# Kernel tuning notes

Hardware: AMD Instinct MI355X
Metric: run time of the kernel (lower is better)

## Reference

```python
import jax, jax.numpy as jnp
import numpy as np

N_EMBED = 384
N_HEAD = 6
HEAD_SIZE = N_EMBED // N_HEAD  # 64
LN_EPS = 1e-5


def setup_inputs() -> dict:
    key = jax.random.key(0)
    ks = jax.random.split(key, 12)
    B, T = 128, 256
    s_in = 1.0 / np.sqrt(N_EMBED)
    s_ff = 1.0 / np.sqrt(4 * N_EMBED)
    return {
        "x": jax.random.normal(ks[0], (B, T, N_EMBED), jnp.float32),
        "Wq": jax.random.normal(ks[1], (N_HEAD, N_EMBED, HEAD_SIZE), jnp.float32) * s_in,
        "Wk": jax.random.normal(ks[2], (N_HEAD, N_EMBED, HEAD_SIZE), jnp.float32) * s_in,
        "Wv": jax.random.normal(ks[3], (N_HEAD, N_EMBED, HEAD_SIZE), jnp.float32) * s_in,
        "Wproj": jax.random.normal(ks[4], (N_EMBED, N_EMBED), jnp.float32) * s_in,
        "bproj": jnp.zeros((N_EMBED,), jnp.float32),
        "W1": jax.random.normal(ks[5], (N_EMBED, 4 * N_EMBED), jnp.float32) * s_in,
        "b1": jnp.zeros((4 * N_EMBED,), jnp.float32),
        "W2": jax.random.normal(ks[6], (4 * N_EMBED, N_EMBED), jnp.float32) * s_ff,
        "b2": jnp.zeros((N_EMBED,), jnp.float32),
        "ln1_g": jnp.ones((N_EMBED,), jnp.float32),
        "ln1_b": jnp.zeros((N_EMBED,), jnp.float32),
        "ln2_g": jnp.ones((N_EMBED,), jnp.float32),
        "ln2_b": jnp.zeros((N_EMBED,), jnp.float32),
    }


def _layernorm(x, g, b):
    mu = jnp.mean(x, axis=-1, keepdims=True)
    var = jnp.mean(jnp.square(x - mu), axis=-1, keepdims=True)
    return (x - mu) * jax.lax.rsqrt(var + LN_EPS) * g + b


def _attention(xn, Wq, Wk, Wv, Wproj, bproj):
    B, T, C = xn.shape
    q = jnp.einsum("btc,hcd->bhtd", xn, Wq)
    k = jnp.einsum("btc,hcd->bhtd", xn, Wk)
    v = jnp.einsum("btc,hcd->bhtd", xn, Wv)
    # NOTE: original scales by C**-0.5 with C = n_embed (384), not head_size
    scores = jnp.einsum("bhtd,bhsd->bhts", q, k) * (C ** -0.5)
    causal = jnp.tril(jnp.ones((T, T), bool))
    scores = jnp.where(causal, scores, -jnp.inf)
    wei = jax.nn.softmax(scores, axis=-1)
    out = jnp.einsum("bhts,bhsd->bhtd", wei, v)
    out = out.transpose(0, 2, 1, 3).reshape(B, T, N_EMBED)  # concat heads
    return out @ Wproj + bproj


def reference(x, Wq, Wk, Wv, Wproj, bproj, W1, b1, W2, b2, ln1_g, ln1_b, ln2_g, ln2_b):
    x = x + _attention(_layernorm(x, ln1_g, ln1_b), Wq, Wk, Wv, Wproj, bproj)
    h = _layernorm(x, ln2_g, ln2_b)
    ff = jax.nn.relu(h @ W1 + b1) @ W2 + b2
    return x + ff
```

## Files before the change

### kernel.cpp

```cpp
#include <hip/hip_runtime.h>
#include <hip/hip_bf16.h>

typedef __hip_bfloat16 bf16;
typedef __attribute__((ext_vector_type(8))) short bf16x8;
typedef __attribute__((ext_vector_type(4))) float f32x4;

#define CEMB 384
#define NHEAD 6
#define HSZ 64
#define TSEQ 256
#define BATCH 128
#define MROWS (BATCH*TSEQ)
#define FDIM 1536
#define QSCALE 0.05103103630798288f
#define SMAX 8.0f

#define AS1 __attribute__((address_space(1)))
#define AS3 __attribute__((address_space(3)))
__device__ __forceinline__ void gload16(const void* g, void* l){
  __builtin_amdgcn_global_load_lds((const AS1 unsigned*)(g), (AS3 unsigned*)(l), 16, 0, 0);
}

__global__ __launch_bounds__(256) void ln_kernel(const float* __restrict__ x,
    const float* __restrict__ gam, const float* __restrict__ bet,
    bf16* __restrict__ y)
{
  const int row  = blockIdx.x*4 + (threadIdx.x>>6);
  const int lane = threadIdx.x & 63;
  const float* xr = x + (size_t)row*CEMB;
  float v[6]; float s = 0.f;
  #pragma unroll
  for (int i=0;i<6;i++){ v[i] = xr[lane + i*64]; s += v[i]; }
  #pragma unroll
  for (int m=1;m<64;m<<=1) s += __shfl_xor(s, m, 64);
  const float mu = s * (1.0f/CEMB);
  float qs = 0.f;
  #pragma unroll
  for (int i=0;i<6;i++){ v[i] -= mu; qs += v[i]*v[i]; }
  #pragma unroll
  for (int m=1;m<64;m<<=1) qs += __shfl_xor(qs, m, 64);
  const float rs = rsqrtf(qs*(1.0f/CEMB) + 1e-5f);
  bf16* yr = y + (size_t)row*CEMB;
  #pragma unroll
  for (int i=0;i<6;i++){
    int c = lane + i*64;
    yr[c] = __float2bfloat16(v[i]*rs*gam[c] + bet[c]);
  }
}

__global__ __launch_bounds__(256) void transpose_to_bf16(const float* __restrict__ src,
    bf16* __restrict__ dst, int K, int N)
{
  __shared__ float tile[32][33];
  const int n0 = blockIdx.x*32, k0 = blockIdx.y*32;
  src += (size_t)blockIdx.z*K*N;
  dst += (size_t)blockIdx.z*K*N;
  const int c = threadIdx.x & 31, r8 = threadIdx.x >> 5;
  #pragma unroll
  for (int i=0;i<4;i++)
    tile[r8 + i*8][c] = src[(size_t)(k0 + r8 + i*8)*N + n0 + c];
  __syncthreads();
  #pragma unroll
  for (int i=0;i<4;i++)
    dst[(size_t)(n0 + r8 + i*8)*K + k0 + c] = __float2bfloat16(tile[c][r8 + i*8]);
}

__global__ __launch_bounds__(256) void transpose_qkv(const float* __restrict__ Wq,
    const float* __restrict__ Wk, const float* __restrict__ Wv, bf16* __restrict__ dst)
{
  __shared__ float tile[32][33];
  const int z = blockIdx.z;
  const float* src = (z < 6) ? Wq : (z < 12 ? Wk : Wv);
  src += (size_t)(z % 6) * CEMB * HSZ;
  dst += (size_t)z * CEMB * HSZ;
  const int n0 = blockIdx.x*32, k0 = blockIdx.y*32;
  const int c = threadIdx.x & 31, r8 = threadIdx.x >> 5;
  #pragma unroll
  for (int i=0;i<4;i++)
    tile[r8 + i*8][c] = src[(size_t)(k0 + r8 + i*8)*HSZ + n0 + c];
  __syncthreads();
  #pragma unroll
  for (int i=0;i<4;i++)
    dst[(size_t)(n0 + r8 + i*8)*CEMB + k0 + c] = __float2bfloat16(tile[c][r8 + i*8]);
}

template<int EPI, int NN, int NK>
__global__ __launch_bounds__(512) void gemm2(
    const bf16* __restrict__ A, const bf16* __restrict__ BT,
    const float* __restrict__ bias, const float* __restrict__ resid,
    float* __restrict__ outf, bf16* __restrict__ outb0,
    bf16* __restrict__ outb1, bf16* __restrict__ outb2)
{
  constexpr int K = NK*32;
  constexpr int N = NN*128;
  __shared__ char lA[2][256*64];
  __shared__ char lB[2][128*64];
  const int cpx = gridDim.x >> 3;
  const int wg  = (blockIdx.x & 7)*cpx + (blockIdx.x >> 3);
  const int bm = (wg / NN)*256, bn = (wg % NN)*128;
  const int t = threadIdx.x, lane = t & 63, wid = t >> 6;
  const int wr = (wid>>1)*64, wc = (wid&1)*64;
  const int g = lane >> 4, fr = lane & 15;
  const size_t rowK2 = (size_t)K*2;
  f32x4 acc[4][4] = {};

  auto stage = [&](int buf, int kt){
    const size_t ko = (size_t)kt*64;
    #pragma unroll
    for (int i=0;i<2;i++){
      int slot = t + i*512;
      int row = slot>>2, blk = slot&3;
      gload16((const char*)A + (size_t)(bm+row)*rowK2 + ko + ((blk ^ ((row>>1)&3))<<4),
              lA[buf] + slot*16);
    }
    {
      int row = t>>2, blk = t&3;
      gload16((const char*)BT + (size_t)(bn+row)*rowK2 + ko + ((blk ^ ((row>>1)&3))<<4),
              lB[buf] + t*16);
    }
  };

  stage(0, 0);
  __syncthreads();
  int cur = 0;
  #pragma unroll 1
  for (int kt=0; kt<NK; ++kt){
    if (kt+1 < NK) stage(cur^1, kt+1);
    bf16x8 af[4], bq[4];
    #pragma unroll
    for (int mi=0;mi<4;mi++){
      int row = wr + mi*16 + fr;
      af[mi] = *(const bf16x8*)(lA[cur] + row*64 + ((g ^ ((row>>1)&3))<<4));
    }
    #pragma unroll
    for (int nj=0;nj<4;nj++){
      int row = wc + nj*16 + fr;
      bq[nj] = *(const bf16x8*)(lB[cur] + row*64 + ((g ^ ((row>>1)&3))<<4));
    }
    __builtin_amdgcn_s_setprio(1);
    #pragma unroll
    for (int mi=0;mi<4;mi++)
      #pragma unroll
      for (int nj=0;nj<4;nj++)
        acc[mi][nj] = __builtin_amdgcn_mfma_f32_16x16x32_bf16(af[mi], bq[nj], acc[mi][nj], 0, 0, 0);
    __builtin_amdgcn_s_setprio(0);
    __syncthreads();
    cur ^= 1;
  }

  if constexpr (EPI==0){
    const int sel = bn/CEMB;
    bf16* dst = sel==0 ? outb0 : (sel==1 ? outb1 : outb2);
    const float sc = sel==0 ? QSCALE : 1.0f;
    const int nb = bn - sel*CEMB;
    #pragma unroll
    for (int nj=0;nj<4;nj++){
      const int nn = nb + wc + nj*16 + fr;
      const int hh = nn>>6, dd = nn&63;
      #pragma unroll
      for (int mi=0;mi<4;mi++){
        const int m0 = bm + wr + mi*16 + 4*g;
        const int bb = m0>>8, tt0 = m0&255;
        bf16* p = dst + ((size_t)(bb*NHEAD + hh)*TSEQ + tt0)*HSZ + dd;
        #pragma unroll
        for (int e=0;e<4;e++)
          p[(size_t)e*HSZ] = __float2bfloat16(acc[mi][nj][e]*sc);
      }
    }
  } else {
    #pragma unroll
    for (int mi=0;mi<4;mi++)
      #pragma unroll
      for (int nj=0;nj<4;nj++)
        #pragma unroll
        for (int e=0;e<4;e++){
          const int m = bm + wr + mi*16 + 4*g + e;
          const int n = bn + wc + nj*16 + fr;
          const float vacc = acc[mi][nj][e];
          if constexpr (EPI==1 || EPI==3){
            outf[(size_t)m*N + n] = vacc + bias[n] + resid[(size_t)m*N + n];
          } else {
            float z = vacc + bias[n];
            outb0[(size_t)m*N + n] = __float2bfloat16(z > 0.f ? z : 0.f);
          }
        }
  }
}

__global__ __launch_bounds__(256) void attn_kernel(
    const bf16* __restrict__ q, const bf16* __restrict__ k,
    const bf16* __restrict__ v, bf16* __restrict__ out)
{
  __shared__ char kt_lds[64*128];
  __shared__ char vt_lds[80*128];
  __shared__ char p_lds[4][64*128];
  const int bh = blockIdx.x;
  const int bidx = bh / NHEAD, hidx = bh - bidx*NHEAD;
  const int t = threadIdx.x, lane = t & 63, w = t >> 6;
  const int g = lane >> 4, fr = lane & 15;
  const int lrow = lane >> 3;
  const int scol = ((lane & 7) ^ lrow) << 4;
  const size_t base = (size_t)bh * TSEQ * HSZ;

  if (t < 128){
    unsigned int ones2 = 0x3F803F80u;
    uint4 vv;
    if ((t>>3) == 0) vv = uint4{ones2, ones2, ones2, ones2};
    else             vv = uint4{0u, 0u, 0u, 0u};
    *(uint4*)(vt_lds + (64 + (t>>3))*128 + (t&7)*16) = vv;
  }

  bf16x8 qf[4][2];
  #pragma unroll
  for (int mi=0;mi<4;mi++)
    #pragma unroll
    for (int ks=0;ks<2;ks++)
      qf[mi][ks] = *(const bf16x8*)(q + base + (size_t)(w*64 + mi*16 + fr)*HSZ + ks*32 + g*8);

  f32x4 of[4][5] = {};

  for (int j=0;j<4;j++){
    __syncthreads();
    #pragma unroll
    for (int i=0;i<2;i++){
      int r0 = w*16 + i*8;
      gload16((const char*)(k + base + (size_t)(j*64 + r0 + lrow)*HSZ) + scol,
              kt_lds + r0*128);
    }
    #pragma unroll
    for (int i=0;i<2;i++){
      int chunk = t + i*256, r = chunk>>3, c = chunk&7;
      uint4 vv = *(const uint4*)(v + base + (size_t)(j*64 + r)*HSZ + c*8);
      const unsigned short* pv = (const unsigned short*)&vv;
      #pragma unroll
      for (int u=0;u<8;u++)
        *(unsigned short*)(vt_lds + (c*8+u)*128 + ((((r>>3) ^ u ^ c)&7)<<4) + (r&7)*2) = pv[u];
    }
    __syncthreads();
    if (j <= w){
      f32x4 sa[4][4] = {};
      #pragma unroll
      for (int ks=0;ks<2;ks++){
        bf16x8 kf[4];
        #pragma unroll
        for (int nj=0;nj<4;nj++)
          kf[nj] = *(const bf16x8*)(kt_lds + (nj*16+fr)*128 + (((ks*4+g)*16) ^ ((fr&7)<<4)));
        __builtin_amdgcn_s_setprio(1);
        #pragma unroll
        for (int mi=0;mi<4;mi++)
          #pragma unroll
          for (int nj=0;nj<4;nj++)
            sa[mi][nj] = __builtin_amdgcn_mfma_f32_16x16x32_bf16(qf[mi][ks], kf[nj], sa[mi][nj], 0, 0, 0);
        __builtin_amdgcn_s_setprio(0);
      }
      if (j == w){
        #pragma unroll
        for (int mi=0;mi<4;mi++)
          #pragma unroll
          for (int nj=0;nj<4;nj++)
            #pragma unroll
            for (int e=0;e<4;e++)
              if (nj*16 + fr > mi*16 + 4*g + e) sa[mi][nj][e] = -1e30f;
      }
      char* pl = p_lds[w];
      #pragma unroll
      for (int mi=0;mi<4;mi++)
        #pragma unroll
        for (int nj=0;nj<4;nj++)
          #pragma unroll
          for (int e=0;e<4;e++){
            int row = mi*16 + 4*g + e, col = nj*16 + fr;
            float p = __expf(sa[mi][nj][e] - SMAX);
            *(bf16*)(pl + row*128 + (((col>>3) ^ (row&7))<<4) + (col&7)*2) =
                __float2bfloat16(p);
          }
      #pragma unroll
      for (int ks=0;ks<2;ks++){
        bf16x8 pa[4], vf[5];
        #pragma unroll
        for (int mi=0;mi<4;mi++)
          pa[mi] = *(const bf16x8*)(pl + (mi*16+fr)*128 + (((ks*4+g)*16) ^ ((fr&7)<<4)));
        #pragma unroll
        for (int nd=0;nd<5;nd++){
          int d = nd*16 + fr;
          vf[nd] = *(const bf16x8*)(vt_lds + d*128 +
                   ((((ks*4+g) ^ (d&7) ^ ((d>>3)&7))&7)<<4));
        }
        __builtin_amdgcn_s_setprio(1);
        #pragma unroll
        for (int mi=0;mi<4;mi++)
          #pragma unroll
          for (int nd=0;nd<5;nd++)
            of[mi][nd] = __builtin_amdgcn_mfma_f32_16x16x32_bf16(pa[mi], vf[nd], of[mi][nd], 0, 0, 0);
        __builtin_amdgcn_s_setprio(0);
      }
    }
  }
  #pragma unroll
  for (int mi=0;mi<4;mi++){
    float rl[4];
    #pragma unroll
    for (int e=0;e<4;e++){
      float l = __shfl(of[mi][4][e], (int)(lane & 48), 64);
      rl[e] = 1.0f / l;
    }
    #pragma unroll
    for (int nd=0;nd<4;nd++)
      #pragma unroll
      for (int e=0;e<4;e++){
        int row = w*64 + mi*16 + 4*g + e;
        int d = nd*16 + fr;
        out[(size_t)(bidx*TSEQ + row)*CEMB + hidx*HSZ + d] =
            __float2bfloat16(of[mi][nd][e] * rl[e]);
      }
  }
}

extern "C" void kernel_launch(void* const* d_in, const int* in_sizes, int n_in,
                              void* d_out, int out_size, void* d_ws, size_t ws_size,
                              hipStream_t stream)
{
  const float* x     = (const float*)d_in[0];
  const float* Wq    = (const float*)d_in[1];
  const float* Wk    = (const float*)d_in[2];
  const float* Wv    = (const float*)d_in[3];
  const float* Wproj = (const float*)d_in[4];
  const float* bproj = (const float*)d_in[5];
  const float* W1    = (const float*)d_in[6];
  const float* b1    = (const float*)d_in[7];
  const float* W2    = (const float*)d_in[8];
  const float* b2    = (const float*)d_in[9];
  const float* ln1g  = (const float*)d_in[10];
  const float* ln1b  = (const float*)d_in[11];
  const float* ln2g  = (const float*)d_in[12];
  const float* ln2b  = (const float*)d_in[13];

  char* ws = (char*)d_ws;
  const size_t SA = (size_t)MROWS*CEMB*2;
  bf16* xn1    = (bf16*)(ws + 0*SA);
  bf16* qb     = (bf16*)(ws + 1*SA);
  bf16* kbuf   = (bf16*)(ws + 2*SA);
  bf16* vb     = (bf16*)(ws + 3*SA);
  bf16* attn_o = (bf16*)(ws + 0*SA);
  bf16* act    = (bf16*)(ws + 0*SA);
  bf16* hb     = (bf16*)(ws + 4*SA);
  float* x1    = (float*)(ws + 5*SA);
  char* wb     = ws + 5*SA + (size_t)MROWS*CEMB*4;
  bf16* qkvT   = (bf16*)wb;
  bf16* projT  = (bf16*)(wb + (size_t)1152*384*2);
  bf16* w1T    = (bf16*)(wb + (size_t)(1152+384)*384*2);
  bf16* w2T    = (bf16*)(wb + (size_t)(1152+384+1536)*384*2);

  dim3 blk(256), blk5(512);
  transpose_qkv<<<dim3(2,12,18), blk, 0, stream>>>(Wq, Wk, Wv, qkvT);
  transpose_to_bf16<<<dim3(12,12,1), blk, 0, stream>>>(Wproj, projT, CEMB, CEMB);
  transpose_to_bf16<<<dim3(48,12,1), blk, 0, stream>>>(W1,    w1T,   CEMB, FDIM);
  transpose_to_bf16<<<dim3(12,48,1), blk, 0, stream>>>(W2,    w2T,   FDIM, CEMB);

  ln_kernel<<<dim3(MROWS/4), blk, 0, stream>>>(x, ln1g, ln1b, xn1);
  gemm2<0,9,12><<<dim3(1152), blk5, 0, stream>>>(xn1, qkvT, nullptr, nullptr,
                                                 nullptr, qb, kbuf, vb);
  attn_kernel<<<dim3(768), blk, 0, stream>>>(qb, kbuf, vb, attn_o);
  gemm2<1,3,12><<<dim3(384), blk5, 0, stream>>>(attn_o, projT, bproj, x,
                                                x1, nullptr, nullptr, nullptr);
  ln_kernel<<<dim3(MROWS/4), blk, 0, stream>>>(x1, ln2g, ln2b, hb);
  gemm2<2,12,12><<<dim3(1536), blk5, 0, stream>>>(hb, w1T, b1, nullptr,
                                                  nullptr, act, nullptr, nullptr);
  gemm2<3,3,48><<<dim3(384), blk5, 0, stream>>>(act, w2T, b2, x1,
                                                (float*)d_out, nullptr, nullptr, nullptr);
}
```

Measured before the change: 267.9 us.

## Add 256x256-tile GEMM with split-K-phase LDS pipeline for QKV, proj, FFN1

Introduces a new GEMM kernel with 256x256 output tiles and 8 waves, each computing 128x64. It uses a 128KB double-buffered LDS loaded by direct global-to-LDS loads, interleaving prefetch of the next K-slab with MFMA groups under explicit barriers and waitcnts. The QKV, projection and FFN1 GEMMs switch to it, with N padded to a multiple of 256 and padded columns masked in the epilogue. The aim is more operand reuse per LDS byte and better overlap of loads with MFMA. In exchange, the projection GEMM does wasted work on padding, the large LDS footprint limits occupancy, and the epilogue stores are less coalesced.

```diff
diff --git a/kernel.cpp b/kernel.cpp
--- a/kernel.cpp
+++ b/kernel.cpp
@@ -84,12 +84,133 @@
     dst[(size_t)(n0 + r8 + i*8)*CEMB + k0 + c] = __float2bfloat16(tile[c][r8 + i*8]);
 }
 
-template<int EPI, int NN, int NK>
-__global__ __launch_bounds__(512) void gemm2(
+template<int EPI, int NREAL, int NPAD, int NK>
+__global__ __launch_bounds__(512, 2) void gemm8p(
     const bf16* __restrict__ A, const bf16* __restrict__ BT,
     const float* __restrict__ bias, const float* __restrict__ resid,
     float* __restrict__ outf, bf16* __restrict__ outb0,
     bf16* __restrict__ outb1, bf16* __restrict__ outb2)
+{
+  constexpr int K = NK*64;
+  constexpr int NT = NPAD/256;
+  __shared__ char lds[131072];
+  const int cpx = gridDim.x >> 3;
+  const int wg  = (blockIdx.x & 7)*cpx + (blockIdx.x >> 3);
+  const int bm = (wg / NT)*256, bn = (wg % NT)*256;
+  const int t = threadIdx.x, lane = t & 63, wid = t >> 6;
+  const int wm = wid >> 2, wn = wid & 3;
+  const int g = lane >> 4, fr = lane & 15;
+  const size_t rowb = (size_t)K*2;
+  const int sblk = ((t&3) ^ ((t>>3)&3)) << 4;
+  const int swz  = (g ^ ((fr>>1)&3)) << 4;
+  f32x4 acc[8][4] = {};
+
+  const char* Ag = (const char*)A  + (size_t)(bm + (t>>2))*rowb + sblk;
+  const char* Bg = (const char*)BT + (size_t)(bn + (t>>2))*rowb + sblk;
+  const size_t rstep = rowb*128;
+
+  auto stg = [&](int X, int KH, int sl, int kt2){
+    const char* src = (X ? Bg : Ag) + (size_t)kt2*128 + KH*64;
+    char* dst = lds + X*65536 + (KH*2+sl)*16384 + wid*1024;
+    gload16(src,         dst);
+    gload16(src + rstep, dst + 8192);
+  };
+  auto rdA = [&](bf16x8* af, int sl, int MH, int KS){
+    const char* p = lds + (KS*2+sl)*16384 + (wm*128 + MH*64 + fr)*64 + swz;
+    #pragma unroll
+    for (int mi=0;mi<4;mi++) af[mi] = *(const bf16x8*)(p + mi*1024);
+  };
+  auto rdB = [&](bf16x8* bq, int sl, int KS){
+    const char* p = lds + 65536 + (KS*2+sl)*16384 + (wn*64 + fr)*64 + swz;
+    #pragma unroll
+    for (int nj=0;nj<4;nj++) bq[nj] = *(const bf16x8*)(p + nj*1024);
+  };
+
+#define MFMA16(MH) \
+  __builtin_amdgcn_s_setprio(1); \
+  _Pragma("unroll") \
+  for (int mi=0;mi<4;mi++){ \
+    _Pragma("unroll") \
+    for (int nj=0;nj<4;nj++) \
+      acc[(MH)*4+mi][nj] = __builtin_amdgcn_mfma_f32_16x16x32_bf16(af[mi], bq[nj], acc[(MH)*4+mi][nj], 0, 0, 0); \
+  } \
+  __builtin_amdgcn_s_setprio(0);
+
+  stg(0,0,0,0); stg(1,0,0,0); stg(0,1,0,0); stg(1,1,0,0);
+  asm volatile("s_waitcnt vmcnt(4)" ::: "memory");
+  __builtin_amdgcn_s_barrier();
+
+  #pragma unroll 1
+  for (int kt=0; kt<NK; ++kt){
+    const int sl = kt&1, sn = sl^1;
+    const bool pf = (kt+1 < NK);
+    bf16x8 af[4], bq[4];
+    rdA(af, sl, 0, 0); rdB(bq, sl, 0);
+    if (pf) stg(0,0,sn,kt+1);
+    __builtin_amdgcn_s_barrier();
+    asm volatile("s_waitcnt lgkmcnt(0)" ::: "memory");
+    __builtin_amdgcn_sched_barrier(0);
+    MFMA16(0)
+    __builtin_amdgcn_s_barrier();
+    rdA(af, sl, 1, 0);
+    if (pf){ stg(1,0,sn,kt+1);
+             asm volatile("s_waitcnt vmcnt(4)" ::: "memory"); }
+    else     asm volatile("s_waitcnt vmcnt(0)" ::: "memory");
+    __builtin_amdgcn_s_barrier();
+    asm volatile("s_waitcnt lgkmcnt(0)" ::: "memory");
+    __builtin_amdgcn_sched_barrier(0);
+    MFMA16(1)
+    __builtin_amdgcn_s_barrier();
+    rdA(af, sl, 0, 1); rdB(bq, sl, 1);
+    if (pf) stg(0,1,sn,kt+1);
+    __builtin_amdgcn_s_barrier();
+    asm volatile("s_waitcnt lgkmcnt(0)" ::: "memory");
+    __builtin_amdgcn_sched_barrier(0);
+    MFMA16(0)
+    __builtin_amdgcn_s_barrier();
+    rdA(af, sl, 1, 1);
+    if (pf){ stg(1,1,sn,kt+1);
+             asm volatile("s_waitcnt vmcnt(4)" ::: "memory"); }
+    __builtin_amdgcn_s_barrier();
+    asm volatile("s_waitcnt lgkmcnt(0)" ::: "memory");
+    __builtin_amdgcn_sched_barrier(0);
+    MFMA16(1)
+    __builtin_amdgcn_s_barrier();
+  }
+#undef MFMA16
+
+  #pragma unroll
+  for (int mi=0;mi<8;mi++)
+    #pragma unroll
+    for (int nj=0;nj<4;nj++)
+      #pragma unroll
+      for (int e=0;e<4;e++){
+        const int m = bm + wm*128 + mi*16 + 4*g + e;
+        const int n = bn + wn*64 + nj*16 + fr;
+        if (NPAD == NREAL || n < NREAL){
+          const float vacc = acc[mi][nj][e];
+          if constexpr (EPI==0){
+            int sel = n/CEMB; int nn = n - sel*CEMB;
+            int hh = nn>>6, dd = nn&63;
+            int bb = m>>8,  tt = m&255;
+            bf16 val = __float2bfloat16(sel==0 ? vacc * QSCALE : vacc);
+            bf16* dst = sel==0 ? outb0 : (sel==1 ? outb1 : outb2);
+            dst[((size_t)(bb*NHEAD + hh)*TSEQ + tt)*HSZ + dd] = val;
+          } else if constexpr (EPI==1){
+            outf[(size_t)m*NREAL + n] = vacc + bias[n] + resid[(size_t)m*NREAL + n];
+          } else {
+            float z = vacc + bias[n];
+            outb0[(size_t)m*NREAL + n] = __float2bfloat16(z > 0.f ? z : 0.f);
+          }
+        }
+      }
+}
+
+template<int EPI, int NN, int NK>
+__global__ __launch_bounds__(512) void gemm3(
+    const bf16* __restrict__ A, const bf16* __restrict__ BT,
+    const float* __restrict__ bias, const float* __restrict__ resid,
+    float* __restrict__ outf)
 {
   constexpr int K = NK*32;
   constexpr int N = NN*128;
@@ -147,44 +268,16 @@
     __syncthreads();
     cur ^= 1;
   }
-
-  if constexpr (EPI==0){
-    const int sel = bn/CEMB;
-    bf16* dst = sel==0 ? outb0 : (sel==1 ? outb1 : outb2);
-    const float sc = sel==0 ? QSCALE : 1.0f;
-    const int nb = bn - sel*CEMB;
-    #pragma unroll
-    for (int nj=0;nj<4;nj++){
-      const int nn = nb + wc + nj*16 + fr;
-      const int hh = nn>>6, dd = nn&63;
-      #pragma unroll
-      for (int mi=0;mi<4;mi++){
-        const int m0 = bm + wr + mi*16 + 4*g;
-        const int bb = m0>>8, tt0 = m0&255;
-        bf16* p = dst + ((size_t)(bb*NHEAD + hh)*TSEQ + tt0)*HSZ + dd;
-        #pragma unroll
-        for (int e=0;e<4;e++)
-          p[(size_t)e*HSZ] = __float2bfloat16(acc[mi][nj][e]*sc);
-      }
-    }
-  } else {
-    #pragma unroll
-    for (int mi=0;mi<4;mi++)
-      #pragma unroll
-      for (int nj=0;nj<4;nj++)
-        #pragma unroll
-        for (int e=0;e<4;e++){
-          const int m = bm + wr + mi*16 + 4*g + e;
-          const int n = bn + wc + nj*16 + fr;
-          const float vacc = acc[mi][nj][e];
-          if constexpr (EPI==1 || EPI==3){
-            outf[(size_t)m*N + n] = vacc + bias[n] + resid[(size_t)m*N + n];
-          } else {
-            float z = vacc + bias[n];
-            outb0[(size_t)m*N + n] = __float2bfloat16(z > 0.f ? z : 0.f);
-          }
-        }
-  }
+  #pragma unroll
+  for (int mi=0;mi<4;mi++)
+    #pragma unroll
+    for (int nj=0;nj<4;nj++)
+      #pragma unroll
+      for (int e=0;e<4;e++){
+        const int m = bm + wr + mi*16 + 4*g + e;
+        const int n = bn + wc + nj*16 + fr;
+        outf[(size_t)m*N + n] = acc[mi][nj][e] + bias[n] + resid[(size_t)m*N + n];
+      }
 }
 
 __global__ __launch_bounds__(256) void attn_kernel(
@@ -347,9 +440,9 @@
   float* x1    = (float*)(ws + 5*SA);
   char* wb     = ws + 5*SA + (size_t)MROWS*CEMB*4;
   bf16* qkvT   = (bf16*)wb;
-  bf16* projT  = (bf16*)(wb + (size_t)1152*384*2);
-  bf16* w1T    = (bf16*)(wb + (size_t)(1152+384)*384*2);
-  bf16* w2T    = (bf16*)(wb + (size_t)(1152+384+1536)*384*2);
+  bf16* projT  = (bf16*)(wb + (size_t)1280*384*2);
+  bf16* w1T    = (bf16*)(wb + (size_t)(1280+512)*384*2);
+  bf16* w2T    = (bf16*)(wb + (size_t)(1280+512+1536)*384*2);
 
   dim3 blk(256), blk5(512);
   transpose_qkv<<<dim3(2,12,18), blk, 0, stream>>>(Wq, Wk, Wv, qkvT);
@@ -358,14 +451,13 @@
   transpose_to_bf16<<<dim3(12,48,1), blk, 0, stream>>>(W2,    w2T,   FDIM, CEMB);
 
   ln_kernel<<<dim3(MROWS/4), blk, 0, stream>>>(x, ln1g, ln1b, xn1);
-  gemm2<0,9,12><<<dim3(1152), blk5, 0, stream>>>(xn1, qkvT, nullptr, nullptr,
-                                                 nullptr, qb, kbuf, vb);
+  gemm8p<0,1152,1280,6><<<dim3(640), blk5, 0, stream>>>(xn1, qkvT, nullptr, nullptr,
+                                                        nullptr, qb, kbuf, vb);
   attn_kernel<<<dim3(768), blk, 0, stream>>>(qb, kbuf, vb, attn_o);
-  gemm2<1,3,12><<<dim3(384), blk5, 0, stream>>>(attn_o, projT, bproj, x,
-                                                x1, nullptr, nullptr, nullptr);
+  gemm8p<1,384,512,6><<<dim3(256), blk5, 0, stream>>>(attn_o, projT, bproj, x,
+                                                      x1, nullptr, nullptr, nullptr);
   ln_kernel<<<dim3(MROWS/4), blk, 0, stream>>>(x1, ln2g, ln2b, hb);
-  gemm2<2,12,12><<<dim3(1536), blk5, 0, stream>>>(hb, w1T, b1, nullptr,
-                                                  nullptr, act, nullptr, nullptr);
-  gemm2<3,3,48><<<dim3(384), blk5, 0, stream>>>(act, w2T, b2, x1,
-                                                (float*)d_out, nullptr, nullptr, nullptr);
-}
+  gemm8p<2,1536,1536,6><<<dim3(768), blk5, 0, stream>>>(hb, w1T, b1, nullptr,
+                                                        nullptr, act, nullptr, nullptr);
+  gemm3<3,3,48><<<dim3(384), blk5, 0, stream>>>(act, w2T, b2, x1, (float*)d_out);
+}
```

After: 276.6 us. +3.3%, slower.
